# Kernel optimization log

Measured on AMD Instinct MI355X. Metric: run time of the kernel, lower is better.

## Reference

```python
import jax, jax.numpy as jnp
import numpy as np

D_MODEL = 512

def setup_inputs() -> dict:
    key = jax.random.key(0)
    ks = jax.random.split(key, 7)
    B, C, H, W = 16, D_MODEL, 64, 64
    x = jax.random.normal(ks[0], (B, C, H, W), dtype=jnp.float32)
    s = 1.0 / np.sqrt(C)
    Wq = jax.random.normal(ks[1], (C, C), dtype=jnp.float32) * s
    bq = jax.random.normal(ks[2], (C,), dtype=jnp.float32) * 0.01
    Wk = jax.random.normal(ks[3], (C, C), dtype=jnp.float32) * s
    bk = jax.random.normal(ks[4], (C,), dtype=jnp.float32) * 0.01
    Wv = jax.random.normal(ks[5], (C, C), dtype=jnp.float32) * s
    bv = jax.random.normal(ks[6], (C,), dtype=jnp.float32) * 0.01
    return {"x": x, "Wq": Wq, "bq": bq, "Wk": Wk, "bk": bk, "Wv": Wv, "bv": bv}

def reference(x, Wq, bq, Wk, bk, Wv, bv):
    B, C, H, W = x.shape
    N = H * W
    xf = x.reshape(B, C, N)  # flatten spatial
    # 1x1 conv == per-position channel matmul: out[b,o,n] = W[o,c] x[b,c,n] + b[o]
    q = jnp.einsum('oc,bcn->bon', Wq, xf) + bq[None, :, None]
    k = jnp.einsum('oc,bcn->bon', Wk, xf) + bk[None, :, None]
    v = jnp.einsum('oc,bcn->bon', Wv, xf) + bv[None, :, None]
    # channel-attention: attn is [B, C, C]
    attn = jnp.einsum('bcn,bdn->bcd', q, k) / jnp.sqrt(jnp.asarray(C, x.dtype))
    attn = jax.nn.softmax(attn, axis=-1)
    out = jnp.einsum('bcd,bdn->bcn', attn, v)
    return out.reshape(B, C, H, W)
```

## Files before the change

kernel.cpp:

```cpp
#include <hip/hip_runtime.h>
#include <cstdint>

typedef _Float16 f16;
typedef f16 f16x4 __attribute__((ext_vector_type(4)));
typedef f16 f16x8 __attribute__((ext_vector_type(8)));
typedef float f32x4 __attribute__((ext_vector_type(4)));

typedef __attribute__((address_space(1))) void gvoid_t;
typedef __attribute__((address_space(3))) void lvoid_t;

__device__ __forceinline__ void gload_lds16(const void* g, void* l) {
    __builtin_amdgcn_global_load_lds((gvoid_t*)const_cast<void*>(g),
                                     (lvoid_t*)l, 16, 0, 0);
}

template<int EPI>
__global__ __launch_bounds__(256) void gemm64_nt(
    const f16* __restrict__ A, const f16* __restrict__ B, void* __restrict__ Cv,
    int M, int N, int K, long long sA, long long sB, long long sC)
{
    const int b = blockIdx.z;
    __shared__ alignas(16) f16 As[64 * 32];
    __shared__ alignas(16) f16 Bs[64 * 32];

    const int tid  = threadIdx.x;
    const int wave = tid >> 6;
    const int lane = tid & 63;
    const int quad = lane >> 4;
    const int l16  = lane & 15;

    const int m0 = blockIdx.x * 64;
    const int n0 = blockIdx.y * 64;
    const int wm = (wave >> 1) * 32;
    const int wn = (wave & 1) * 32;

    const f16* Ag = A + (long long)b * sA + (long long)(m0 + (tid >> 2)) * K + (tid & 3) * 8;
    const f16* Bg = B + (long long)b * sB + (long long)(n0 + (tid >> 2)) * K + (tid & 3) * 8;
    f16* Asl = &As[tid * 8];
    f16* Bsl = &Bs[tid * 8];

    f32x4 acc[2][2] = {};

    for (int kk = 0; kk < K; kk += 32) {
        gload_lds16(Ag, Asl);
        gload_lds16(Bg, Bsl);
        Ag += 32; Bg += 32;
        __syncthreads();

        f16x8 af[2], bf[2];
        #pragma unroll
        for (int i = 0; i < 2; i++)
            af[i] = *reinterpret_cast<const f16x8*>(&As[(wm + i * 16 + l16) * 32 + quad * 8]);
        #pragma unroll
        for (int j = 0; j < 2; j++)
            bf[j] = *reinterpret_cast<const f16x8*>(&Bs[(wn + j * 16 + l16) * 32 + quad * 8]);
        #pragma unroll
        for (int i = 0; i < 2; i++)
            #pragma unroll
            for (int j = 0; j < 2; j++)
                acc[i][j] = __builtin_amdgcn_mfma_f32_16x16x32_f16(af[i], bf[j], acc[i][j], 0, 0, 0);
        __syncthreads();
    }

    #pragma unroll
    for (int i = 0; i < 2; i++)
        #pragma unroll
        for (int j = 0; j < 2; j++)
            #pragma unroll
            for (int r = 0; r < 4; r++) {
                const int row = m0 + wm + i * 16 + quad * 4 + r;
                const int col = n0 + wn + j * 16 + l16;
                const long long idx = (long long)b * sC + (long long)row * N + col;
                if constexpr (EPI == 0) ((f16*)Cv)[idx] = (f16)acc[i][j][r];
                else                    ((float*)Cv)[idx] = acc[i][j][r];
            }
}

__global__ __launch_bounds__(256) void gemm128_bias(
    const f16* __restrict__ A, const f16* __restrict__ B, float* __restrict__ C,
    const float* __restrict__ rowbias,
    int M, int N, int K, long long sA, long long sB, long long sC)
{
    const int b = blockIdx.z;
    __shared__ alignas(16) f16 As[128 * 32];
    __shared__ alignas(16) f16 Bs[128 * 32];

    const int tid  = threadIdx.x;
    const int wave = tid >> 6;
    const int lane = tid & 63;
    const int quad = lane >> 4;
    const int l16  = lane & 15;

    const int m0 = blockIdx.x * 128;
    const int n0 = blockIdx.y * 128;
    const int wm = (wave >> 1) * 64;
    const int wn = (wave & 1) * 64;

    const f16* Ag = A + (long long)b * sA + (long long)(m0 + (tid >> 2)) * K + (tid & 3) * 8;
    const f16* Bg = B + (long long)b * sB + (long long)(n0 + (tid >> 2)) * K + (tid & 3) * 8;
    f16* Asl = &As[tid * 8];
    f16* Bsl = &Bs[tid * 8];
    const long long rowskip = 64LL * K;

    f32x4 acc[4][4] = {};

    for (int kk = 0; kk < K; kk += 32) {
        gload_lds16(Ag,           Asl);
        gload_lds16(Ag + rowskip, Asl + 2048);
        gload_lds16(Bg,           Bsl);
        gload_lds16(Bg + rowskip, Bsl + 2048);
        Ag += 32; Bg += 32;
        __syncthreads();

        f16x8 af[4], bf[4];
        #pragma unroll
        for (int i = 0; i < 4; i++)
            af[i] = *reinterpret_cast<const f16x8*>(&As[(wm + i * 16 + l16) * 32 + quad * 8]);
        #pragma unroll
        for (int j = 0; j < 4; j++)
            bf[j] = *reinterpret_cast<const f16x8*>(&Bs[(wn + j * 16 + l16) * 32 + quad * 8]);
        #pragma unroll
        for (int i = 0; i < 4; i++)
            #pragma unroll
            for (int j = 0; j < 4; j++)
                acc[i][j] = __builtin_amdgcn_mfma_f32_16x16x32_f16(af[i], bf[j], acc[i][j], 0, 0, 0);
        __syncthreads();
    }

    #pragma unroll
    for (int i = 0; i < 4; i++)
        #pragma unroll
        for (int j = 0; j < 4; j++)
            #pragma unroll
            for (int r = 0; r < 4; r++) {
                const int row = m0 + wm + i * 16 + quad * 4 + r;
                const int col = n0 + wn + j * 16 + l16;
                const long long idx = (long long)b * sC + (long long)row * N + col;
                C[idx] = acc[i][j][r] + rowbias[(long long)b * M + row];
            }
}

__global__ __launch_bounds__(256) void transpose_cast_x(
    const float* __restrict__ x, f16* __restrict__ xh, f16* __restrict__ xT,
    float* __restrict__ r)
{
    __shared__ float t[64][65];
    const int b  = blockIdx.z;
    const int n0 = blockIdx.x * 64;
    const int c0 = blockIdx.y * 64;
    const int cg = threadIdx.x & 15;
    const int cr = threadIdx.x >> 4;

    const float* xb  = x  + ((long long)b * 512 + c0) * 4096 + n0;
    f16*         xhb = xh + ((long long)b * 512 + c0) * 4096 + n0;

    #pragma unroll
    for (int s = 0; s < 64; s += 16) {
        const int row = cr + s;
        const float4 ld = *reinterpret_cast<const float4*>(&xb[(long long)row * 4096 + cg * 4]);
        f16x4 h; h[0] = (f16)ld.x; h[1] = (f16)ld.y; h[2] = (f16)ld.z; h[3] = (f16)ld.w;
        *reinterpret_cast<f16x4*>(&xhb[(long long)row * 4096 + cg * 4]) = h;
        t[row][cg * 4 + 0] = ld.x; t[row][cg * 4 + 1] = ld.y;
        t[row][cg * 4 + 2] = ld.z; t[row][cg * 4 + 3] = ld.w;
        float sm = ld.x + ld.y + ld.z + ld.w;
        sm += __shfl_xor(sm, 1, 64); sm += __shfl_xor(sm, 2, 64);
        sm += __shfl_xor(sm, 4, 64); sm += __shfl_xor(sm, 8, 64);
        if (cg == 0) atomicAdd(&r[b * 512 + c0 + row], sm);
    }
    __syncthreads();
    f16* xTb = xT + ((long long)b * 4096 + n0) * 512 + c0;
    #pragma unroll
    for (int s = 0; s < 64; s += 16) {
        const int nr = cr + s;
        f16x4 h;
        h[0] = (f16)t[cg * 4 + 0][nr]; h[1] = (f16)t[cg * 4 + 1][nr];
        h[2] = (f16)t[cg * 4 + 2][nr]; h[3] = (f16)t[cg * 4 + 3][nr];
        *reinterpret_cast<f16x4*>(&xTb[(long long)nr * 512 + cg * 4]) = h;
    }
}

__global__ __launch_bounds__(256) void cast_w4(
    const float* __restrict__ W, f16* __restrict__ o)
{
    const int i = blockIdx.x * 256 + threadIdx.x;
    const float4 ld = reinterpret_cast<const float4*>(W)[i];
    f16x4 h; h[0] = (f16)ld.x; h[1] = (f16)ld.y; h[2] = (f16)ld.z; h[3] = (f16)ld.w;
    reinterpret_cast<f16x4*>(o)[i] = h;
}

__global__ __launch_bounds__(256) void transpose_cast_w(
    const float* __restrict__ W, f16* __restrict__ WT)
{
    __shared__ float t[32][33];
    const int r0 = blockIdx.y * 32, c0 = blockIdx.x * 32;
    const int tx = threadIdx.x & 31, ty = threadIdx.x >> 5;
    #pragma unroll
    for (int i = 0; i < 32; i += 8)
        t[ty + i][tx] = W[(long long)(r0 + ty + i) * 512 + c0 + tx];
    __syncthreads();
    #pragma unroll
    for (int i = 0; i < 32; i += 8)
        WT[(long long)(c0 + ty + i) * 512 + r0 + tx] = (f16)t[tx][ty + i];
}

__global__ __launch_bounds__(256) void matvec_u(
    const float* __restrict__ Wq, const float* __restrict__ Wk,
    const float* __restrict__ r, float* __restrict__ u1, float* __restrict__ u2)
{
    const int w = blockIdx.x * 4 + (threadIdx.x >> 6);
    const int lane = threadIdx.x & 63;
    const int which = w >> 13;
    const int b = (w >> 9) & 15;
    const int i = w & 511;
    const float* W = which ? Wk : Wq;
    const float* rb = r + b * 512;
    float s = 0.f;
    #pragma unroll
    for (int j = 0; j < 8; j++) {
        const int c = lane + 64 * j;
        s += W[(long long)i * 512 + c] * rb[c];
    }
    #pragma unroll
    for (int off = 32; off > 0; off >>= 1) s += __shfl_xor(s, off, 64);
    if (lane == 0) (which ? u2 : u1)[b * 512 + i] = s;
}

__global__ __launch_bounds__(256) void softmax_bias(
    const float* __restrict__ S, const float* __restrict__ bq,
    const float* __restrict__ bk, const float* __restrict__ bv,
    const float* __restrict__ u1, const float* __restrict__ u2,
    f16* __restrict__ attn, float* __restrict__ rowbias)
{
    const int wave = threadIdx.x >> 6;
    const int lane = threadIdx.x & 63;
    const long long row = (long long)blockIdx.x * 4 + wave;
    const int b = (int)(row >> 9);
    const int c = (int)(row & 511);
    const float* src = S + row * 512;
    const float u1c = u1[row];
    const float bqc = bq[c];
    const float scale = 0.04419417382415922f;

    float v[8], bkv[8];
    float mx = -1e30f;
    #pragma unroll
    for (int j = 0; j < 8; j++) {
        const int d = lane + 64 * j;
        bkv[j] = bk[d];
        float val = src[d] + u1c * bkv[j] + bqc * u2[b * 512 + d] + 4096.0f * bqc * bkv[j];
        val *= scale;
        v[j] = val;
        mx = fmaxf(mx, val);
    }
    #pragma unroll
    for (int off = 32; off > 0; off >>= 1) mx = fmaxf(mx, __shfl_xor(mx, off, 64));
    float sum = 0.f;
    #pragma unroll
    for (int j = 0; j < 8; j++) { v[j] = __expf(v[j] - mx); sum += v[j]; }
    #pragma unroll
    for (int off = 32; off > 0; off >>= 1) sum += __shfl_xor(sum, off, 64);
    const float inv = 1.0f / sum;

    float rb_ = 0.f;
    f16* dst = attn + row * 512;
    #pragma unroll
    for (int j = 0; j < 8; j++) {
        const int d = lane + 64 * j;
        const float p = v[j] * inv;
        dst[d] = (f16)p;
        rb_ += p * bv[d];
    }
    #pragma unroll
    for (int off = 32; off > 0; off >>= 1) rb_ += __shfl_xor(rb_, off, 64);
    if (lane == 0) rowbias[row] = rb_;
}

extern "C" void kernel_launch(void* const* d_in, const int* in_sizes, int n_in,
                              void* d_out, int out_size, void* d_ws, size_t ws_size,
                              hipStream_t stream)
{
    const float* x  = (const float*)d_in[0];
    const float* Wq = (const float*)d_in[1];
    const float* bq = (const float*)d_in[2];
    const float* Wk = (const float*)d_in[3];
    const float* bk = (const float*)d_in[4];
    const float* Wv = (const float*)d_in[5];
    const float* bv = (const float*)d_in[6];
    float* out = (float*)d_out;

    const int B = 16, C = 512, N = 4096;
    const long long CN = (long long)C * N;
    const long long CC = (long long)C * C;

    char* ws = (char*)d_ws;
    size_t off = 0;
    auto alloc = [&](size_t bytes) -> void* {
        void* p = ws + off;
        off += (bytes + 255) & ~(size_t)255;
        return p;
    };
    f16*   xh   = (f16*)  alloc((size_t)B * CN * 2);
    f16*   xT   = (f16*)  alloc((size_t)B * CN * 2);
    f16*   G    = (f16*)  alloc((size_t)B * CC * 2);
    f16*   T    = (f16*)  alloc((size_t)B * CC * 2);
    float* S    = (float*)alloc((size_t)B * CC * 4);
    f16*   attn = (f16*)  alloc((size_t)B * CC * 2);
    f16*   U    = (f16*)  alloc((size_t)B * CC * 2);
    f16*   Wqh  = (f16*)  alloc((size_t)CC * 2);
    f16*   Wkh  = (f16*)  alloc((size_t)CC * 2);
    f16*   WvT  = (f16*)  alloc((size_t)CC * 2);
    float* r    = (float*)alloc((size_t)B * C * 4);
    float* u1   = (float*)alloc((size_t)B * C * 4);
    float* u2   = (float*)alloc((size_t)B * C * 4);
    float* rwb  = (float*)alloc((size_t)B * C * 4);
    (void)ws_size;

    hipMemsetAsync(r, 0, (size_t)B * C * 4, stream);

    transpose_cast_x<<<dim3(N / 64, C / 64, B), 256, 0, stream>>>(x, xh, xT, r);
    cast_w4<<<dim3(C * C / 1024), 256, 0, stream>>>(Wq, Wqh);
    cast_w4<<<dim3(C * C / 1024), 256, 0, stream>>>(Wk, Wkh);
    transpose_cast_w<<<dim3(16, 16), 256, 0, stream>>>(Wv, WvT);
    matvec_u<<<dim3(2 * B * C / 4), 256, 0, stream>>>(Wq, Wk, r, u1, u2);

    gemm64_nt<0><<<dim3(8, 8, B), 256, 0, stream>>>(xh, xh, G, C, C, N, CN, CN, CC);
    gemm64_nt<0><<<dim3(8, 8, B), 256, 0, stream>>>(Wqh, G, T, C, C, C, 0LL, CC, CC);
    gemm64_nt<1><<<dim3(8, 8, B), 256, 0, stream>>>(T, Wkh, S, C, C, C, CC, 0LL, CC);
    softmax_bias<<<dim3(B * C / 4), 256, 0, stream>>>(S, bq, bk, bv, u1, u2, attn, rwb);
    gemm64_nt<0><<<dim3(8, 8, B), 256, 0, stream>>>(attn, WvT, U, C, C, C, CC, 0LL, CC);
    gemm128_bias<<<dim3(C / 128, N / 128, B), 256, 0, stream>>>(
        U, xT, out, rwb, C, N, C, CC, CN, CN);
}
```

Baseline: 482.7 us.

## Compute Gram matrix with split-K 128x128 tiles and separate reduction

Replaces the 64x64-tile Gram GEMM (K=4096, 1024 blocks) with a 128x128-tile kernel that splits K into four slices, writing fp32 partials. A separate reduce kernel sums the four partials and casts to fp16. The larger tiles give more data reuse, and the split keeps the block count at 1024. In exchange it adds 64 MB of fp32 partial writes and reads plus an extra launch. It also merges the two weight-cast launches into one.

```diff
diff --git a/kernel.cpp b/kernel.cpp
--- a/kernel.cpp
+++ b/kernel.cpp
@@ -74,6 +74,88 @@
                 if constexpr (EPI == 0) ((f16*)Cv)[idx] = (f16)acc[i][j][r];
                 else                    ((float*)Cv)[idx] = acc[i][j][r];
             }
+}
+
+__global__ __launch_bounds__(256) void gram_splitk(
+    const f16* __restrict__ xh, float* __restrict__ P)
+{
+    const int b     = blockIdx.z >> 2;
+    const int slice = blockIdx.z & 3;
+
+    __shared__ alignas(16) f16 As[128 * 32];
+    __shared__ alignas(16) f16 Bs[128 * 32];
+
+    const int tid  = threadIdx.x;
+    const int wave = tid >> 6;
+    const int lane = tid & 63;
+    const int quad = lane >> 4;
+    const int l16  = lane & 15;
+
+    const int m0 = blockIdx.x * 128;
+    const int n0 = blockIdx.y * 128;
+    const int wm = (wave >> 1) * 64;
+    const int wn = (wave & 1) * 64;
+
+    const f16* base = xh + (long long)b * (512LL * 4096) + slice * 1024;
+    const f16* Ag = base + (long long)(m0 + (tid >> 2)) * 4096 + (tid & 3) * 8;
+    const f16* Bg = base + (long long)(n0 + (tid >> 2)) * 4096 + (tid & 3) * 8;
+    f16* Asl = &As[tid * 8];
+    f16* Bsl = &Bs[tid * 8];
+    const long long rowskip = 64LL * 4096;
+
+    f32x4 acc[4][4] = {};
+
+    for (int kk = 0; kk < 1024; kk += 32) {
+        gload_lds16(Ag,           Asl);
+        gload_lds16(Ag + rowskip, Asl + 2048);
+        gload_lds16(Bg,           Bsl);
+        gload_lds16(Bg + rowskip, Bsl + 2048);
+        Ag += 32; Bg += 32;
+        __syncthreads();
+
+        f16x8 af[4], bf[4];
+        #pragma unroll
+        for (int i = 0; i < 4; i++)
+            af[i] = *reinterpret_cast<const f16x8*>(&As[(wm + i * 16 + l16) * 32 + quad * 8]);
+        #pragma unroll
+        for (int j = 0; j < 4; j++)
+            bf[j] = *reinterpret_cast<const f16x8*>(&Bs[(wn + j * 16 + l16) * 32 + quad * 8]);
+        #pragma unroll
+        for (int i = 0; i < 4; i++)
+            #pragma unroll
+            for (int j = 0; j < 4; j++)
+                acc[i][j] = __builtin_amdgcn_mfma_f32_16x16x32_f16(af[i], bf[j], acc[i][j], 0, 0, 0);
+        __syncthreads();
+    }
+
+    float* Pt = P + ((long long)slice * 16 + b) * (512LL * 512);
+    #pragma unroll
+    for (int i = 0; i < 4; i++)
+        #pragma unroll
+        for (int j = 0; j < 4; j++)
+            #pragma unroll
+            for (int r = 0; r < 4; r++) {
+                const int row = m0 + wm + i * 16 + quad * 4 + r;
+                const int col = n0 + wn + j * 16 + l16;
+                Pt[(long long)row * 512 + col] = acc[i][j][r];
+            }
+}
+
+__global__ __launch_bounds__(256) void reduce_cast(
+    const float* __restrict__ P, f16* __restrict__ G16)
+{
+    const long long i4 = (long long)blockIdx.x * 256 + threadIdx.x;
+    const long long stride4 = 16LL * 512 * 512 / 4;
+    const float4 a = reinterpret_cast<const float4*>(P)[i4];
+    const float4 b = reinterpret_cast<const float4*>(P)[i4 + stride4];
+    const float4 c = reinterpret_cast<const float4*>(P)[i4 + 2 * stride4];
+    const float4 d = reinterpret_cast<const float4*>(P)[i4 + 3 * stride4];
+    f16x4 h;
+    h[0] = (f16)(a.x + b.x + c.x + d.x);
+    h[1] = (f16)(a.y + b.y + c.y + d.y);
+    h[2] = (f16)(a.z + b.z + c.z + d.z);
+    h[3] = (f16)(a.w + b.w + c.w + d.w);
+    reinterpret_cast<f16x4*>(G16)[i4] = h;
 }
 
 __global__ __launch_bounds__(256) void gemm128_bias(
@@ -179,10 +261,14 @@
     }
 }
 
-__global__ __launch_bounds__(256) void cast_w4(
-    const float* __restrict__ W, f16* __restrict__ o)
-{
-    const int i = blockIdx.x * 256 + threadIdx.x;
+__global__ __launch_bounds__(256) void cast_w2(
+    const float* __restrict__ Wq, const float* __restrict__ Wk,
+    f16* __restrict__ oq, f16* __restrict__ ok)
+{
+    const int blk = blockIdx.x;
+    const float* W = (blk < 256) ? Wq : Wk;
+    f16* o = (blk < 256) ? oq : ok;
+    const int i = (blk & 255) * 256 + threadIdx.x;
     const float4 ld = reinterpret_cast<const float4*>(W)[i];
     f16x4 h; h[0] = (f16)ld.x; h[1] = (f16)ld.y; h[2] = (f16)ld.z; h[3] = (f16)ld.w;
     reinterpret_cast<f16x4*>(o)[i] = h;
@@ -301,6 +387,7 @@
     };
     f16*   xh   = (f16*)  alloc((size_t)B * CN * 2);
     f16*   xT   = (f16*)  alloc((size_t)B * CN * 2);
+    float* Gp   = (float*)alloc((size_t)4 * B * CC * 4);
     f16*   G    = (f16*)  alloc((size_t)B * CC * 2);
     f16*   T    = (f16*)  alloc((size_t)B * CC * 2);
     float* S    = (float*)alloc((size_t)B * CC * 4);
@@ -318,12 +405,13 @@
     hipMemsetAsync(r, 0, (size_t)B * C * 4, stream);
 
     transpose_cast_x<<<dim3(N / 64, C / 64, B), 256, 0, stream>>>(x, xh, xT, r);
-    cast_w4<<<dim3(C * C / 1024), 256, 0, stream>>>(Wq, Wqh);
-    cast_w4<<<dim3(C * C / 1024), 256, 0, stream>>>(Wk, Wkh);
+    cast_w2<<<dim3(512), 256, 0, stream>>>(Wq, Wk, Wqh, Wkh);
     transpose_cast_w<<<dim3(16, 16), 256, 0, stream>>>(Wv, WvT);
     matvec_u<<<dim3(2 * B * C / 4), 256, 0, stream>>>(Wq, Wk, r, u1, u2);
 
-    gemm64_nt<0><<<dim3(8, 8, B), 256, 0, stream>>>(xh, xh, G, C, C, N, CN, CN, CC);
+    gram_splitk<<<dim3(4, 4, B * 4), 256, 0, stream>>>(xh, Gp);
+    reduce_cast<<<dim3((unsigned)(B * CC / 4 / 256)), 256, 0, stream>>>(Gp, G);
+
     gemm64_nt<0><<<dim3(8, 8, B), 256, 0, stream>>>(Wqh, G, T, C, C, C, 0LL, CC, CC);
     gemm64_nt<1><<<dim3(8, 8, B), 256, 0, stream>>>(T, Wkh, S, C, C, C, CC, 0LL, CC);
     softmax_bias<<<dim3(B * C / 4), 256, 0, stream>>>(S, bq, bk, bv, u1, u2, attn, rwb);
```

Result: faster. 452.2 us (-6.3%).
